# Performance work log

Measured on AMD Instinct MI355X. Metric: run time of the kernel, lower is better.

The kernel has to match this reference:

```python
import jax, jax.numpy as jnp
import numpy as np

H = 4  # num heads, hard-coded in Encoder's GAT(hidden, hidden, hidden, 4, 2)


def build_adjacency(shot_type, encode_length):
    # Faithful vectorized port of initialize_adjacency_matrix.
    B, S = shot_type.shape
    N = 2 * encode_length
    base = np.zeros((14, N, N), dtype=np.int32)
    base[13] = 1 - np.eye(N, dtype=np.int32)  # complete graph minus self-loops
    for row in range(N):
        ni = row // 2
        if row % 2 == 0:
            col = (ni + 1) * 2
            rel = 11 if ni % 2 == 0 else 12
        else:
            col = (ni + 1) * 2 + 1
            rel = 12 if ni % 2 == 0 else 11
        if col <= N - 1:
            base[rel, row, col] = 1
            base[rel, col, row] = 1
            base[13, row, col] = 0
            base[13, col, row] = 0
    adj = jnp.tile(jnp.asarray(base)[None], (B, 1, 1, 1))  # [B,14,N,N]
    steps = np.arange(S)
    even = steps % 2 == 0
    i = np.where(even, 2 * steps, 2 * steps + 1)
    j = np.where(even, 2 * (steps + 1) + 1, 2 * (steps + 1))
    b = np.broadcast_to(np.arange(B)[:, None], (B, S))
    i = np.broadcast_to(i, (B, S))
    j = np.broadcast_to(j, (B, S))
    adj = adj.at[b, shot_type, i, j].set(1)
    adj = adj.at[b, shot_type, j, i].set(1)
    adj = adj.at[b, 13, i, j].set(0)
    adj = adj.at[b, 13, j, i].set(0)
    return adj


def gat_layer(x, mask, W, att):
    # x: [B,N,in], W: [in, H*F], att: [H, 2F]; standard GAT concat-score,
    # computed as a_src.h_i + a_dst.h_j (== a^T [h_i || h_j]).
    B, N, _ = x.shape
    F = att.shape[1] // 2
    h = (x @ W).reshape(B, N, H, F).transpose(0, 2, 1, 3)       # [B,H,N,F]
    s_src = jnp.einsum('bhnf,hf->bhn', h, att[:, :F])
    s_dst = jnp.einsum('bhnf,hf->bhn', h, att[:, F:])
    scores = s_src[:, :, :, None] + s_dst[:, :, None, :]        # [B,H,N,N]
    scores = jnp.where(scores > 0, scores, 0.2 * scores)        # LeakyReLU(0.2)
    scores = jnp.where(mask[:, None], scores, -jnp.inf)
    attn = jax.nn.softmax(scores, axis=-1)                      # dropout: eval mode
    hp = jnp.einsum('bhij,bhjf->bhif', attn, h)
    return hp.transpose(0, 2, 1, 3).reshape(B, N, H * F)


def setup_inputs() -> dict:
    B, E = 32, 256
    player_num, player_dim, location_dim, hidden = 35, 32, 32, 64
    k = jax.random.split(jax.random.key(0), 16)

    def lin(key, fan_in, shape):
        return jax.random.normal(key, shape, dtype=jnp.float32) / np.sqrt(fan_in)

    return {
        'player': jax.random.randint(k[0], (B, 2), 0, player_num),
        'shot_type': jax.random.randint(k[1], (B, E - 1), 0, 11),
        'player_A_x': jax.random.uniform(k[2], (B, E), dtype=jnp.float32),
        'player_A_y': jax.random.uniform(k[3], (B, E), dtype=jnp.float32),
        'player_B_x': jax.random.uniform(k[4], (B, E), dtype=jnp.float32),
        'player_B_y': jax.random.uniform(k[5], (B, E), dtype=jnp.float32),
        'encode_length': E,
        'emb_table': jax.random.normal(k[6], (player_num, player_dim), dtype=jnp.float32),
        'Wc': lin(k[7], 2, (2, location_dim)),
        'bc': jnp.zeros((location_dim,), dtype=jnp.float32),
        'Wm': lin(k[8], player_dim + location_dim, (player_dim + location_dim, hidden)),
        'bm': jnp.zeros((hidden,), dtype=jnp.float32),
        'lin1_W': lin(k[9], hidden, (hidden, H * hidden)),
        'att1': lin(k[10], 2 * hidden, (H, 2 * hidden)),
        'lin2_W': lin(k[11], H * hidden, (H * hidden, H * hidden)),
        'att2': lin(k[12], 2 * hidden, (H, 2 * hidden)),
    }


def reference(player, shot_type, player_A_x, player_A_y, player_B_x, player_B_y,
              encode_length, emb_table, Wc, bc, Wm, bm, lin1_W, att1, lin2_W, att2):
    E = int(encode_length)
    B = player.shape[0]
    adj = build_adjacency(shot_type, E)                 # [B,14,N,N]
    mask = adj.sum(axis=1) > 0                          # union over relations [B,N,N]
    coord_A = jnp.stack([player_A_x, player_A_y], axis=-1)   # [B,E,2]
    coord_B = jnp.stack([player_B_x, player_B_y], axis=-1)
    coord = jnp.stack([coord_A, coord_B], axis=2).reshape(B, -1, 2)  # [B,2E,2]
    ct = jax.nn.relu(coord @ Wc + bc)                   # [B,2E,loc]
    p = jnp.tile(player, (1, E))                        # [B,2E]
    pe = emb_table[p]                                   # [B,2E,pdim]
    x = jnp.concatenate([ct, pe], axis=-1) @ Wm + bm    # [B,2E,hidden]
    x = jax.nn.relu(gat_layer(x, mask, lin1_W, att1))
    node_embedding = gat_layer(x, mask, lin2_W, att2)   # [B,2E,H*hidden]
    return node_embedding, adj
```

## Files before the change

kernel.cpp:

```cpp
#include <hip/hip_runtime.h>
#include <hip/hip_bf16.h>
#include <stdint.h>

static constexpr int B_  = 32;
static constexpr int E_  = 256;
static constexpr int N_  = 512;
static constexpr int C_  = 256;
static constexpr int BN  = B_ * N_;
static constexpr int NODE_ELEMS = B_ * N_ * C_;
static constexpr int ADJ_ELEMS  = B_ * 14 * N_ * N_;

#define LOG2E 1.44269504088896340736f

typedef __attribute__((ext_vector_type(8))) short v8bf;
typedef __attribute__((ext_vector_type(4))) float v4f;

__device__ __forceinline__ unsigned short f2bfbits(float f) {
  union { float f; unsigned u; } x; x.f = f;
  unsigned u = x.u;
  return (unsigned short)((u + 0x7FFFu + ((u >> 16) & 1u)) >> 16);
}

struct ConvArgs {
  const void* src[15];
  void* dst[15];
  int n[15];
  int kind[15];
};

__global__ __launch_bounds__(256) void k_conv2(ConvArgs a, const unsigned* fprobe,
                                               const unsigned* iprobe) {
  __shared__ int fk_s, ik_s;
  int t = threadIdx.x;
  if (t == 0) {
    int c_even = 0, c_lo = 0;
    for (int k = 0; k < 32; ++k) {
      unsigned w = fprobe[2 * k];
      unsigned e32 = (w >> 23) & 0xFFu;
      unsigned elo = (w >> 7) & 0xFFu;
      if (e32 >= 105u && e32 <= 135u) ++c_even;
      if (elo >= 105u && elo <= 135u) ++c_lo;
    }
    fk_s = (c_even < 16) ? 2 : ((c_lo >= 16) ? 1 : 0);
    int hi0 = 0;
    for (int k = 0; k < 32; ++k) if (iprobe[2 * k + 1] == 0u) ++hi0;
    ik_s = (hi0 >= 30) ? 1 : 0;
  }
  __syncthreads();
  int fk = fk_s, ik = ik_s;
  int arr = blockIdx.y;
  int n = a.n[arr], kind = a.kind[arr];
  for (int idx = blockIdx.x * 256 + t; idx < n; idx += gridDim.x * 256) {
    if (kind == 0) {
      float v;
      if (fk == 2) {
        v = (float)((const double*)a.src[arr])[idx];
      } else if (fk == 1) {
        unsigned short u = ((const unsigned short*)a.src[arr])[idx];
        union { unsigned u; float f; } c; c.u = (unsigned)u << 16; v = c.f;
      } else {
        v = ((const float*)a.src[arr])[idx];
      }
      ((float*)a.dst[arr])[idx] = v;
    } else {
      int v;
      if (ik == 1) v = (int)((const long long*)a.src[arr])[idx];
      else         v = ((const int*)a.src[arr])[idx];
      ((int*)a.dst[arr])[idx] = v;
    }
  }
}

__global__ __launch_bounds__(64) void k_feat2(
    const int* __restrict__ player, const float* __restrict__ Ax, const float* __restrict__ Ay,
    const float* __restrict__ Bx, const float* __restrict__ By,
    const float* __restrict__ emb, const float* __restrict__ Wc, const float* __restrict__ bc,
    const float* __restrict__ Wm, const float* __restrict__ bm, float* __restrict__ x) {
  int id = blockIdx.x * 64 + threadIdx.x;
  if (id >= BN) return;
  int b = id >> 9, n = id & 511;
  int e = n >> 1, side = n & 1;
  float cx = side ? Bx[b * E_ + e] : Ax[b * E_ + e];
  float cy = side ? By[b * E_ + e] : Ay[b * E_ + e];
  int pid = player[b * 2 + side];
  float ct[32];
  for (int k = 0; k < 32; ++k)
    ct[k] = fmaxf(fmaf(cx, Wc[k], fmaf(cy, Wc[32 + k], bc[k])), 0.f);
  for (int o = 0; o < 64; ++o) {
    float acc = bm[o];
    for (int c = 0; c < 32; ++c) acc = fmaf(ct[c], Wm[c * 64 + o], acc);
    for (int c = 0; c < 32; ++c) acc = fmaf(emb[pid * 32 + c], Wm[(32 + c) * 64 + o], acc);
    x[(size_t)id * 64 + o] = acc;
  }
}

__global__ __launch_bounds__(256) void k_gemm(
    const float* __restrict__ x, const float* __restrict__ W, float* __restrict__ h, int K,
    const float* __restrict__ att, float* __restrict__ ssO, float* __restrict__ sdO) {
  __shared__ float xs[64 * 64];
  __shared__ float wt[64 * 64];
  int row0 = blockIdx.x * 64;
  int col0 = blockIdx.y * 64;
  int hd = blockIdx.y;
  int t = threadIdx.x;
  int tx = t & 15, ty = t >> 4;
  float acc[4][4] = {};
  for (int kt = 0; kt < K; kt += 64) {
    #pragma unroll
    for (int q = 0; q < 4; ++q) {
      int v = q * 256 + t;
      int r = v >> 4, c = (v & 15) * 4;
      *(float4*)&xs[r * 64 + c] = *(const float4*)&x[(size_t)(row0 + r) * K + kt + c];
      *(float4*)&wt[r * 64 + c] = *(const float4*)&W[(size_t)(kt + r) * C_ + col0 + c];
    }
    __syncthreads();
    #pragma unroll 4
    for (int k = 0; k < 64; ++k) {
      float xv[4];
      #pragma unroll
      for (int r = 0; r < 4; ++r) xv[r] = xs[(ty * 4 + r) * 64 + k];
      float4 wf = *(const float4*)&wt[k * 64 + tx * 4];
      #pragma unroll
      for (int r = 0; r < 4; ++r) {
        acc[r][0] = fmaf(xv[r], wf.x, acc[r][0]);
        acc[r][1] = fmaf(xv[r], wf.y, acc[r][1]);
        acc[r][2] = fmaf(xv[r], wf.z, acc[r][2]);
        acc[r][3] = fmaf(xv[r], wf.w, acc[r][3]);
      }
    }
    __syncthreads();
  }
  #pragma unroll
  for (int r = 0; r < 4; ++r) {
    int row = row0 + ty * 4 + r;
    float4 o = make_float4(acc[r][0], acc[r][1], acc[r][2], acc[r][3]);
    *(float4*)&h[(size_t)row * C_ + col0 + tx * 4] = o;
  }
  float attS[4], attD[4];
  #pragma unroll
  for (int c = 0; c < 4; ++c) {
    attS[c] = att[hd * 128 + tx * 4 + c];
    attD[c] = att[hd * 128 + 64 + tx * 4 + c];
  }
  #pragma unroll
  for (int r = 0; r < 4; ++r) {
    float p1 = acc[r][0] * attS[0] + acc[r][1] * attS[1] + acc[r][2] * attS[2] + acc[r][3] * attS[3];
    float p2 = acc[r][0] * attD[0] + acc[r][1] * attD[1] + acc[r][2] * attD[2] + acc[r][3] * attD[3];
    #pragma unroll
    for (int d = 8; d > 0; d >>= 1) {
      p1 += __shfl_xor(p1, d, 16);
      p2 += __shfl_xor(p2, d, 16);
    }
    if (tx == 0) {
      int row = row0 + ty * 4 + r;
      int bb = row >> 9, nn = row & 511;
      int idx = (bb * 4 + hd) * N_ + nn;
      ssO[idx] = p1; sdO[idx] = p2;
    }
  }
}

template <int RELU>
__global__ __launch_bounds__(256) void k_attn_mfma2(
    const float* __restrict__ h, const float* __restrict__ ss, const float* __restrict__ sd,
    float* __restrict__ outf) {
  __shared__ unsigned short hs[64 * 72];
  __shared__ float sdl[512];
  __shared__ float red[4];
  __shared__ float ls[4][32];
  int blk = blockIdx.x;
  int it = blk & 3, hd = (blk >> 2) & 3, b = blk >> 4;
  int i0 = it * 128, bh = b * 4 + hd;
  int t = threadIdx.x, w = t >> 6, l = t & 63;
  int lane16 = l & 15, quad = l >> 4;
  float v0 = sd[(size_t)bh * N_ + t];
  float v1 = sd[(size_t)bh * N_ + 256 + t];
  sdl[t] = v0; sdl[256 + t] = v1;
  float mx = fmaxf(v0, v1);
  #pragma unroll
  for (int d = 32; d > 0; d >>= 1) mx = fmaxf(mx, __shfl_xor(mx, d, 64));
  if (l == 0) red[w] = mx;
  __syncthreads();
  mx = fmaxf(fmaxf(red[0], red[1]), fmaxf(red[2], red[3]));
  float ss_s[2], m2_s[2], lsum[2] = {0.f, 0.f};
  #pragma unroll
  for (int s = 0; s < 2; ++s) {
    int i = i0 + w * 32 + s * 16 + lane16;
    ss_s[s] = ss[(size_t)bh * N_ + i];
    float sv = ss_s[s] + mx;
    m2_s[s] = fmaxf(sv, 0.2f * sv) * LOG2E;
  }
  v4f acc[2][4] = {};
  for (int jt = 0; jt < 8; ++jt) {
    int j0 = jt * 64;
    #pragma unroll
    for (int q = 0; q < 4; ++q) {
      int v = q * 256 + t;
      int j = v >> 4, f0 = (v & 15) * 4;
      float4 hv = *(const float4*)&h[(size_t)(b * N_ + j0 + j) * C_ + hd * 64 + f0];
      hs[(f0 + 0) * 72 + j] = f2bfbits(hv.x);
      hs[(f0 + 1) * 72 + j] = f2bfbits(hv.y);
      hs[(f0 + 2) * 72 + j] = f2bfbits(hv.z);
      hs[(f0 + 3) * 72 + j] = f2bfbits(hv.w);
    }
    __syncthreads();
    #pragma unroll
    for (int ks = 0; ks < 2; ++ks) {
      int kb = ks * 32;
      v8bf afr[2];
      #pragma unroll
      for (int s = 0; s < 2; ++s) {
        int i = i0 + w * 32 + s * 16 + lane16;
        #pragma unroll
        for (int q = 0; q < 8; ++q) {
          int j = j0 + kb + quad * 8 + q;
          float sv = ss_s[s] + sdl[j];
          float sc = fmaxf(sv, 0.2f * sv);
          float p = exp2f(fmaf(sc, LOG2E, -m2_s[s]));
          if (i == j) p = 0.f;
          lsum[s] += p;
          afr[s][q] = (short)f2bfbits(p);
        }
      }
      #pragma unroll
      for (int fs = 0; fs < 4; ++fs) {
        v8bf bfr = *(const v8bf*)&hs[(fs * 16 + lane16) * 72 + kb + quad * 8];
        acc[0][fs] = __builtin_amdgcn_mfma_f32_16x16x32_bf16(afr[0], bfr, acc[0][fs], 0, 0, 0);
        acc[1][fs] = __builtin_amdgcn_mfma_f32_16x16x32_bf16(afr[1], bfr, acc[1][fs], 0, 0, 0);
      }
    }
    __syncthreads();
  }
  #pragma unroll
  for (int s = 0; s < 2; ++s) {
    lsum[s] += __shfl_xor(lsum[s], 16, 64);
    lsum[s] += __shfl_xor(lsum[s], 32, 64);
    if (quad == 0) ls[w][s * 16 + lane16] = lsum[s];
  }
  __syncthreads();
  #pragma unroll
  for (int s = 0; s < 2; ++s) {
    #pragma unroll
    for (int r = 0; r < 4; ++r) {
      int i = i0 + w * 32 + s * 16 + quad * 4 + r;
      float scale = 1.f / ls[w][s * 16 + quad * 4 + r];
      #pragma unroll
      for (int fs = 0; fs < 4; ++fs) {
        int f = fs * 16 + lane16;
        float vv = acc[s][fs][r] * scale;
        if constexpr (RELU) vv = fmaxf(vv, 0.f);
        outf[(size_t)(b * N_ + i) * C_ + hd * 64 + f] = vv;
      }
    }
  }
}

__global__ __launch_bounds__(256) void k_adjf2(
    const int* __restrict__ st, float* __restrict__ adj) {
  int chunk = blockIdx.x * 256 + threadIdx.x;
  int j0 = (chunk & 127) << 2;
  int rowid = chunk >> 7;
  int i = rowid & 511;
  int plane = rowid >> 9;
  int r = plane % 14;
  int b = plane / 14;
  float vals[4];
  #pragma unroll
  for (int q = 0; q < 4; ++q) {
    int j = j0 + q;
    int d = j - i;
    int ad = d < 0 ? -d : d;
    int mn = d < 0 ? j : i;
    int m4 = mn & 3;
    float v = 0.f;
    if (r == 13) {
      bool excl = (d == 0) || (ad == 2) || (ad == 3 && m4 == 0) || (ad == 1 && m4 == 3);
      v = excl ? 0.f : 1.f;
    } else if (r == 11) {
      v = (ad == 2 && (m4 == 0 || m4 == 3)) ? 1.f : 0.f;
    } else if (r == 12) {
      v = (ad == 2 && (m4 == 1 || m4 == 2)) ? 1.f : 0.f;
    } else {
      bool sp = (ad == 3 && m4 == 0) || (ad == 1 && m4 == 3);
      if (sp) v = (st[b * 255 + (mn >> 1)] == r) ? 1.f : 0.f;
    }
    vals[q] = v;
  }
  *(float4*)&adj[(size_t)chunk * 4] = make_float4(vals[0], vals[1], vals[2], vals[3]);
}

__global__ __launch_bounds__(256) void k_adjf(
    const unsigned* __restrict__ st_raw, float* __restrict__ adj) {
  __shared__ int i64_s;
  if (threadIdx.x == 0) {
    int hi0 = 0;
    for (int k = 0; k < 32; ++k) if (st_raw[2 * k + 1] == 0u) ++hi0;
    i64_s = (hi0 >= 30) ? 1 : 0;
  }
  __syncthreads();
  int is64 = i64_s;
  int chunk = blockIdx.x * 256 + threadIdx.x;
  int j0 = (chunk & 127) << 2;
  int rowid = chunk >> 7;
  int i = rowid & 511;
  int plane = rowid >> 9;
  int r = plane % 14;
  int b = plane / 14;
  float vals[4];
  #pragma unroll
  for (int q = 0; q < 4; ++q) {
    int j = j0 + q;
    int d = j - i;
    int ad = d < 0 ? -d : d;
    int mn = d < 0 ? j : i;
    int m4 = mn & 3;
    float v = 0.f;
    if (r == 13) {
      bool excl = (d == 0) || (ad == 2) || (ad == 3 && m4 == 0) || (ad == 1 && m4 == 3);
      v = excl ? 0.f : 1.f;
    } else if (r == 11) {
      v = (ad == 2 && (m4 == 0 || m4 == 3)) ? 1.f : 0.f;
    } else if (r == 12) {
      v = (ad == 2 && (m4 == 1 || m4 == 2)) ? 1.f : 0.f;
    } else {
      bool sp = (ad == 3 && m4 == 0) || (ad == 1 && m4 == 3);
      if (sp) {
        int e = b * 255 + (mn >> 1);
        int stv = is64 ? (int)st_raw[2 * e] : (int)st_raw[e];
        v = (stv == r) ? 1.f : 0.f;
      }
    }
    vals[q] = v;
  }
  *(float4*)&adj[(size_t)chunk * 4] = make_float4(vals[0], vals[1], vals[2], vals[3]);
}

__global__ void k_sentinel(float* out, float v) {
  if (threadIdx.x == 0 && blockIdx.x == 0) out[0] = v;
}

extern "C" void kernel_launch(void* const* d_in, const int* in_sizes, int n_in,
                              void* d_out, int out_size, void* d_ws, size_t ws_size,
                              hipStream_t stream) {
  static const int expA[16] = {64,8160,8192,8192,8192,8192,1,1120,64,32,4096,64,16384,512,65536,512};
  static const int expB[15] = {64,8160,8192,8192,8192,8192,1120,64,32,4096,64,16384,512,65536,512};
  int mismatch = -1;
  int base = 7;
  if (n_in == 16) {
    base = 7;
    for (int i = 0; i < 16; ++i) if (in_sizes[i] != expA[i]) { mismatch = i; break; }
  } else if (n_in == 15) {
    base = 6;
    for (int i = 0; i < 15; ++i) if (in_sizes[i] != expB[i]) { mismatch = i; break; }
  } else {
    mismatch = 17;
  }
  if (mismatch < 0 && out_size != NODE_ELEMS + ADJ_ELEMS) mismatch = 16;

  float* out_node = (float*)d_out;
  float* out_adjf = out_node + NODE_ELEMS;

  char* scr = (char*)out_adjf;
  float* x  = (float*)(scr);
  float* h  = (float*)(scr + (size_t)( 4u << 20));
  float* x2 = (float*)(scr + (size_t)(24u << 20));
  float* ss = (float*)(scr + (size_t)(44u << 20));
  float* sd = (float*)(scr + (size_t)(45u << 20));
  float* cv = (float*)(scr + (size_t)(48u << 20));

  float* cAx  = cv + 0;
  float* cAy  = cv + 8192;
  float* cBx  = cv + 16384;
  float* cBy  = cv + 24576;
  float* cEmb = cv + 32768;
  float* cWc  = cv + 33888;
  float* cbc  = cv + 33952;
  float* cWm  = cv + 33984;
  float* cbm  = cv + 38080;
  float* cW1  = cv + 38144;
  float* cA1  = cv + 54528;
  float* cW2  = cv + 55040;
  float* cA2  = cv + 120576;
  int*   cPl  = (int*)(cv + 121088);

  bool ws_ok = (ws_size >= 8160 * sizeof(int));
  int* cSt = ws_ok ? (int*)d_ws : nullptr;

  ConvArgs a;
  a.src[0]  = d_in[2];        a.dst[0]  = cAx;  a.n[0]  = 8192;  a.kind[0]  = 0;
  a.src[1]  = d_in[3];        a.dst[1]  = cAy;  a.n[1]  = 8192;  a.kind[1]  = 0;
  a.src[2]  = d_in[4];        a.dst[2]  = cBx;  a.n[2]  = 8192;  a.kind[2]  = 0;
  a.src[3]  = d_in[5];        a.dst[3]  = cBy;  a.n[3]  = 8192;  a.kind[3]  = 0;
  a.src[4]  = d_in[base + 0]; a.dst[4]  = cEmb; a.n[4]  = 1120;  a.kind[4]  = 0;
  a.src[5]  = d_in[base + 1]; a.dst[5]  = cWc;  a.n[5]  = 64;    a.kind[5]  = 0;
  a.src[6]  = d_in[base + 2]; a.dst[6]  = cbc;  a.n[6]  = 32;    a.kind[6]  = 0;
  a.src[7]  = d_in[base + 3]; a.dst[7]  = cWm;  a.n[7]  = 4096;  a.kind[7]  = 0;
  a.src[8]  = d_in[base + 4]; a.dst[8]  = cbm;  a.n[8]  = 64;    a.kind[8]  = 0;
  a.src[9]  = d_in[base + 5]; a.dst[9]  = cW1;  a.n[9]  = 16384; a.kind[9]  = 0;
  a.src[10] = d_in[base + 6]; a.dst[10] = cA1;  a.n[10] = 512;   a.kind[10] = 0;
  a.src[11] = d_in[base + 7]; a.dst[11] = cW2;  a.n[11] = 65536; a.kind[11] = 0;
  a.src[12] = d_in[base + 8]; a.dst[12] = cA2;  a.n[12] = 512;   a.kind[12] = 0;
  a.src[13] = d_in[0];        a.dst[13] = cPl;  a.n[13] = 64;    a.kind[13] = 1;
  a.src[14] = d_in[1];        a.dst[14] = ws_ok ? (void*)cSt : (void*)cPl;
  a.n[14] = ws_ok ? 8160 : 0; a.kind[14] = 1;

  k_conv2<<<dim3(64, 15), 256, 0, stream>>>(a, (const unsigned*)d_in[base + 3],
                                            (const unsigned*)d_in[0]);

  k_feat2<<<BN / 64, 64, 0, stream>>>(cPl, cAx, cAy, cBx, cBy, cEmb, cWc, cbc, cWm, cbm, x);

  k_gemm<<<dim3(BN / 64, 4), 256, 0, stream>>>(x, cW1, h, 64, cA1, ss, sd);
  k_attn_mfma2<1><<<B_ * 4 * (N_ / 128), 256, 0, stream>>>(h, ss, sd, x2);

  k_gemm<<<dim3(BN / 64, 4), 256, 0, stream>>>(x2, cW2, h, 256, cA2, ss, sd);
  k_attn_mfma2<0><<<B_ * 4 * (N_ / 128), 256, 0, stream>>>(h, ss, sd, out_node);

  if (ws_ok) {
    k_adjf2<<<(ADJ_ELEMS / 4) / 256, 256, 0, stream>>>(cSt, out_adjf);
  } else {
    k_adjf<<<(ADJ_ELEMS / 4) / 256, 256, 0, stream>>>((const unsigned*)d_in[1], out_adjf);
  }

  if (mismatch >= 0) {
    float v = ldexpf(1024.f, mismatch);
    k_sentinel<<<1, 64, 0, stream>>>(out_node, v);
  }
}
```

Before: 647.8 us.

## Use bf16 MFMA for second GAT projection with bf16 activations and transposed weights

Replaces the fp32 second-layer projection GEMM with a bf16 MFMA kernel that reads activations written as bf16 by the first attention kernel and a weight matrix transposed and converted to bf16 during the input-conversion pass. The fused attention-score dot products are kept in the new kernel's epilogue. The aim is to cut the FLOP and memory cost of the 16384x256x256 GEMM and halve the intermediate activation traffic. In exchange it adds bf16 rounding error on the layer-2 inputs and weights.

Result: no change. 638.8 us (-1.4%).

```diff
diff --git a/kernel.cpp b/kernel.cpp
--- a/kernel.cpp
+++ b/kernel.cpp
@@ -51,7 +51,12 @@
   int arr = blockIdx.y;
   int n = a.n[arr], kind = a.kind[arr];
   for (int idx = blockIdx.x * 256 + t; idx < n; idx += gridDim.x * 256) {
-    if (kind == 0) {
+    if (kind == 1) {
+      int v;
+      if (ik == 1) v = (int)((const long long*)a.src[arr])[idx];
+      else         v = ((const int*)a.src[arr])[idx];
+      ((int*)a.dst[arr])[idx] = v;
+    } else {
       float v;
       if (fk == 2) {
         v = (float)((const double*)a.src[arr])[idx];
@@ -61,12 +66,12 @@
       } else {
         v = ((const float*)a.src[arr])[idx];
       }
-      ((float*)a.dst[arr])[idx] = v;
-    } else {
-      int v;
-      if (ik == 1) v = (int)((const long long*)a.src[arr])[idx];
-      else         v = ((const int*)a.src[arr])[idx];
-      ((int*)a.dst[arr])[idx] = v;
+      if (kind == 0) {
+        ((float*)a.dst[arr])[idx] = v;
+      } else {
+        int kk = idx >> 8, cc = idx & 255;
+        ((unsigned short*)a.dst[arr])[cc * 256 + kk] = f2bfbits(v);
+      }
     }
   }
 }
@@ -160,10 +165,58 @@
   }
 }
 
+__global__ __launch_bounds__(256) void k_gemm2_mfma(
+    const unsigned short* __restrict__ xb, const unsigned short* __restrict__ wt,
+    float* __restrict__ h, const float* __restrict__ att,
+    float* __restrict__ ssO, float* __restrict__ sdO) {
+  int row0 = blockIdx.x * 64;
+  int col0 = blockIdx.y * 64;
+  int hd = blockIdx.y;
+  int t = threadIdx.x, w = t >> 6, l = t & 63;
+  int lane16 = l & 15, quad = l >> 4;
+  int arow = row0 + w * 16 + lane16;
+  v4f acc[4] = {};
+  #pragma unroll
+  for (int ks = 0; ks < 8; ++ks) {
+    int kb = ks * 32 + quad * 8;
+    v8bf a = *(const v8bf*)&xb[(size_t)arow * 256 + kb];
+    #pragma unroll
+    for (int fs = 0; fs < 4; ++fs) {
+      v8bf b = *(const v8bf*)&wt[(size_t)(col0 + fs * 16 + lane16) * 256 + kb];
+      acc[fs] = __builtin_amdgcn_mfma_f32_16x16x32_bf16(a, b, acc[fs], 0, 0, 0);
+    }
+  }
+  float attS[4], attD[4];
+  #pragma unroll
+  for (int fs = 0; fs < 4; ++fs) {
+    attS[fs] = att[hd * 128 + fs * 16 + lane16];
+    attD[fs] = att[hd * 128 + 64 + fs * 16 + lane16];
+  }
+  #pragma unroll
+  for (int r = 0; r < 4; ++r) {
+    int row = row0 + w * 16 + quad * 4 + r;
+    #pragma unroll
+    for (int fs = 0; fs < 4; ++fs)
+      h[(size_t)row * C_ + col0 + fs * 16 + lane16] = acc[fs][r];
+    float p1 = acc[0][r] * attS[0] + acc[1][r] * attS[1] + acc[2][r] * attS[2] + acc[3][r] * attS[3];
+    float p2 = acc[0][r] * attD[0] + acc[1][r] * attD[1] + acc[2][r] * attD[2] + acc[3][r] * attD[3];
+    #pragma unroll
+    for (int d = 8; d > 0; d >>= 1) {
+      p1 += __shfl_xor(p1, d, 16);
+      p2 += __shfl_xor(p2, d, 16);
+    }
+    if (lane16 == 0) {
+      int bb = row >> 9, nn = row & 511;
+      int idx = (bb * 4 + hd) * N_ + nn;
+      ssO[idx] = p1; sdO[idx] = p2;
+    }
+  }
+}
+
 template <int RELU>
 __global__ __launch_bounds__(256) void k_attn_mfma2(
     const float* __restrict__ h, const float* __restrict__ ss, const float* __restrict__ sd,
-    float* __restrict__ outf) {
+    void* __restrict__ outp) {
   __shared__ unsigned short hs[64 * 72];
   __shared__ float sdl[512];
   __shared__ float red[4];
@@ -248,8 +301,12 @@
       for (int fs = 0; fs < 4; ++fs) {
         int f = fs * 16 + lane16;
         float vv = acc[s][fs][r] * scale;
-        if constexpr (RELU) vv = fmaxf(vv, 0.f);
-        outf[(size_t)(b * N_ + i) * C_ + hd * 64 + f] = vv;
+        size_t o = (size_t)(b * N_ + i) * C_ + hd * 64 + f;
+        if constexpr (RELU) {
+          ((unsigned short*)outp)[o] = f2bfbits(fmaxf(vv, 0.f));
+        } else {
+          ((float*)outp)[o] = vv;
+        }
       }
     }
   }
@@ -363,7 +420,7 @@
   char* scr = (char*)out_adjf;
   float* x  = (float*)(scr);
   float* h  = (float*)(scr + (size_t)( 4u << 20));
-  float* x2 = (float*)(scr + (size_t)(24u << 20));
+  unsigned short* x2b = (unsigned short*)(scr + (size_t)(24u << 20));
   float* ss = (float*)(scr + (size_t)(44u << 20));
   float* sd = (float*)(scr + (size_t)(45u << 20));
   float* cv = (float*)(scr + (size_t)(48u << 20));
@@ -379,7 +436,7 @@
   float* cbm  = cv + 38080;
   float* cW1  = cv + 38144;
   float* cA1  = cv + 54528;
-  float* cW2  = cv + 55040;
+  unsigned short* cW2T = (unsigned short*)(cv + 55040);
   float* cA2  = cv + 120576;
   int*   cPl  = (int*)(cv + 121088);
 
@@ -398,7 +455,7 @@
   a.src[8]  = d_in[base + 4]; a.dst[8]  = cbm;  a.n[8]  = 64;    a.kind[8]  = 0;
   a.src[9]  = d_in[base + 5]; a.dst[9]  = cW1;  a.n[9]  = 16384; a.kind[9]  = 0;
   a.src[10] = d_in[base + 6]; a.dst[10] = cA1;  a.n[10] = 512;   a.kind[10] = 0;
-  a.src[11] = d_in[base + 7]; a.dst[11] = cW2;  a.n[11] = 65536; a.kind[11] = 0;
+  a.src[11] = d_in[base + 7]; a.dst[11] = cW2T; a.n[11] = 65536; a.kind[11] = 2;
   a.src[12] = d_in[base + 8]; a.dst[12] = cA2;  a.n[12] = 512;   a.kind[12] = 0;
   a.src[13] = d_in[0];        a.dst[13] = cPl;  a.n[13] = 64;    a.kind[13] = 1;
   a.src[14] = d_in[1];        a.dst[14] = ws_ok ? (void*)cSt : (void*)cPl;
@@ -410,9 +467,9 @@
   k_feat2<<<BN / 64, 64, 0, stream>>>(cPl, cAx, cAy, cBx, cBy, cEmb, cWc, cbc, cWm, cbm, x);
 
   k_gemm<<<dim3(BN / 64, 4), 256, 0, stream>>>(x, cW1, h, 64, cA1, ss, sd);
-  k_attn_mfma2<1><<<B_ * 4 * (N_ / 128), 256, 0, stream>>>(h, ss, sd, x2);
-
-  k_gemm<<<dim3(BN / 64, 4), 256, 0, stream>>>(x2, cW2, h, 256, cA2, ss, sd);
+  k_attn_mfma2<1><<<B_ * 4 * (N_ / 128), 256, 0, stream>>>(h, ss, sd, x2b);
+
+  k_gemm2_mfma<<<dim3(BN / 64, 4), 256, 0, stream>>>(x2b, cW2T, h, cA2, ss, sd);
   k_attn_mfma2<0><<<B_ * 4 * (N_ / 128), 256, 0, stream>>>(h, ss, sd, out_node);
 
   if (ws_ok) {
```
